# Optimization experiments

Hardware: AMD Instinct MI355X
Metric: run time of the kernel (lower is better)

The kernel has to match this reference:

```python
import jax, jax.numpy as jnp
import numpy as np

V = 25000
E = 100000
NODE_IN = 74
EDGE_IN = 12
OUT = 64
EHID = 128
NUM_STEPS = 6


def setup_inputs() -> dict:
    key = jax.random.key(0)
    ks = jax.random.split(key, 12)
    s = 0.05
    node_feats = jax.random.normal(ks[0], (V, NODE_IN), dtype=jnp.float32)
    edge_feats = jax.random.normal(ks[1], (E, EDGE_IN), dtype=jnp.float32)
    src = jax.random.randint(ks[2], (E,), 0, V)
    dst = jax.random.randint(ks[3], (E,), 0, V)
    # project_node_feats: Linear(node_in, out)
    Wp = jax.random.normal(ks[4], (NODE_IN, OUT), dtype=jnp.float32) * s
    bp = jnp.zeros((OUT,), dtype=jnp.float32)
    # edge network: Linear(edge_in, ehid) -> ReLU -> Linear(ehid, out*out)
    We1 = jax.random.normal(ks[5], (EDGE_IN, EHID), dtype=jnp.float32) * s
    be1 = jnp.zeros((EHID,), dtype=jnp.float32)
    We2 = jax.random.normal(ks[6], (EHID, OUT * OUT), dtype=jnp.float32) * s
    be2 = jnp.zeros((OUT * OUT,), dtype=jnp.float32)
    # NNConv output bias
    bias = jnp.zeros((OUT,), dtype=jnp.float32)
    return {
        "node_feats": node_feats, "edge_feats": edge_feats,
        "src": src, "dst": dst,
        "Wp": Wp, "bp": bp,
        "We1": We1, "be1": be1, "We2": We2, "be2": be2,
        "bias": bias,
    }


def reference(node_feats, edge_feats, src, dst, Wp, bp, We1, be1, We2, be2, bias):
    # project node features
    h = jax.nn.relu(node_feats @ Wp + bp)  # [V, OUT]
    # per-edge weight matrices (same every step -> hoist out of loop)
    ew = jax.nn.relu(edge_feats @ We1 + be1) @ We2 + be2  # [E, OUT*OUT]
    ew = ew.reshape(E, OUT, OUT)
    for _ in range(NUM_STEPS):
        # gather src node feats, batched matvec, scatter-sum to dst
        msg = jnp.einsum('ei,eio->eo', h[src], ew)  # [E, OUT]
        agg = jax.ops.segment_sum(msg, dst, num_segments=V)  # [V, OUT]
        h = jax.nn.relu(agg + bias)
    return h
```

## Files before the change

### kernel.cpp

```cpp
#include <hip/hip_runtime.h>
#include <hip/hip_bf16.h>

#define Vn 25000
#define En 100000
#define NODE_IN 74
#define EDGE_IN 12
#define OUTD 64
#define EHID 128
#define NUM_STEPS 6

#define EPB 64
#define HPAD 68

typedef __attribute__((ext_vector_type(8))) _Float16 half8;
typedef __attribute__((ext_vector_type(16))) float floatx16;

__global__ void proj_kernel(const float* __restrict__ node,
                            const float* __restrict__ Wp,
                            const float* __restrict__ bp,
                            float* __restrict__ h) {
  __shared__ float nf[NODE_IN];
  int v = blockIdx.x;
  int o = threadIdx.x;
  for (int i = o; i < NODE_IN; i += 64) nf[i] = node[(size_t)v * NODE_IN + i];
  __syncthreads();
  float acc = bp[o];
  for (int i = 0; i < NODE_IN; ++i) acc = fmaf(nf[i], Wp[i * OUTD + o], acc);
  h[(size_t)v * OUTD + o] = fmaxf(acc, 0.0f);
}

__global__ void edge_kernel(const float* __restrict__ ef,
                            const float* __restrict__ We1,
                            const float* __restrict__ be1,
                            _Float16* __restrict__ f) {
  __shared__ float es[EDGE_IN];
  int e = blockIdx.x;
  int k = threadIdx.x;
  if (k < EDGE_IN) es[k] = ef[(size_t)e * EDGE_IN + k];
  __syncthreads();
  float acc = be1[k];
  for (int j = 0; j < EDGE_IN; ++j) acc = fmaf(es[j], We1[j * EHID + k], acc);
  f[(size_t)e * EHID + k] = (_Float16)fmaxf(acc, 0.0f);
}

__global__ void w2r_kernel(const float* __restrict__ We2,
                           _Float16* __restrict__ w2s) {
  int g = blockIdx.x * 256 + threadIdx.x;
  int j = g & 7;
  int lane = (g >> 3) & 63;
  int s = (g >> 9) & 7;
  int c = (g >> 12) & 1;
  int i = g >> 13;
  int k = s * 16 + 8 * (lane >> 5) + j;
  int col = i * 64 + c * 32 + (lane & 31);
  w2s[g] = (_Float16)We2[(size_t)k * (OUTD * OUTD) + col];
}

__global__ __launch_bounds__(512) void msg_kernel(
    const float* __restrict__ h,
    const _Float16* __restrict__ f,
    const _Float16* __restrict__ w2s,
    const int* __restrict__ src,
    const int* __restrict__ dst,
    const float* __restrict__ be2,
    float* __restrict__ agg) {
  __shared__ _Float16 h_t[64 * HPAD];
  __shared__ float accbuf[4 * 1024];
  __shared__ int s_dst[EPB];

  const int tid = threadIdx.x;
  const int wvq = tid >> 6;
  const int eh = (wvq >> 2) & 1;
  const int ch = (wvq >> 1) & 1;
  const int kh = wvq & 1;
  const int lane = tid & 63;
  const int l31 = lane & 31;
  const int lh = lane >> 5;
  const int e0 = blockIdx.x * EPB;

  if (tid < EPB) {
    int e = e0 + tid;
    s_dst[tid] = (e < En) ? dst[e] : -1;
  }
  {
    int e = tid & 63;
    int ib = tid >> 6;
    int eg = e0 + e;
    int sv = (eg < En) ? src[eg] : 0;
    const float4* hp = reinterpret_cast<const float4*>(h + (size_t)sv * OUTD + ib * 8);
    for (int cc = 0; cc < 2; ++cc) {
      float4 val = hp[cc];
      int i4 = ib * 8 + cc * 4;
      h_t[(i4 + 0) * HPAD + e] = (_Float16)val.x;
      h_t[(i4 + 1) * HPAD + e] = (_Float16)val.y;
      h_t[(i4 + 2) * HPAD + e] = (_Float16)val.z;
      h_t[(i4 + 3) * HPAD + e] = (_Float16)val.w;
    }
  }
  __syncthreads();

  half8 afr[4];
  {
    int e = e0 + eh * 32 + l31;
    if (e >= En) e = En - 1;
    const _Float16* fr = f + (size_t)e * EHID + kh * 64 + 8 * lh;
    for (int s = 0; s < 4; ++s)
      afr[s] = *reinterpret_cast<const half8*>(fr + s * 16);
  }

  const _Float16* w2b = w2s + ch * 4096 + kh * 2048 + lane * 8;

#define LOADB(dstv, ii)                                                     \
  {                                                                         \
    const _Float16* p_ = w2b + (size_t)(ii) * 8192;                         \
    dstv[0] = *reinterpret_cast<const half8*>(p_);                          \
    dstv[1] = *reinterpret_cast<const half8*>(p_ + 512);                    \
    dstv[2] = *reinterpret_cast<const half8*>(p_ + 1024);                   \
    dstv[3] = *reinterpret_cast<const half8*>(p_ + 1536);                   \
  }

  floatx16 acc = (floatx16){0.f};

  half8 ba[4], bb[4];
  LOADB(ba, 0);
  LOADB(bb, 1);

#define BODY(iv, breg)                                                        \
  {                                                                           \
    _Float16 hh = h_t[(iv) * HPAD + eh * 32 + l31];                           \
    half8 hb = (half8){hh, hh, hh, hh, hh, hh, hh, hh};                       \
    for (int s = 0; s < 4; ++s) {                                             \
      half8 as = afr[s] * hb;                                                 \
      acc = __builtin_amdgcn_mfma_f32_32x32x16_f16(as, breg[s], acc, 0, 0, 0); \
    }                                                                         \
  }

  for (int ii = 0; ii < 32; ++ii) {
    int i0 = 2 * ii;
    BODY(i0, ba);
    {
      int inx = (i0 + 2 < 64) ? i0 + 2 : 63;
      LOADB(ba, inx);
    }
    BODY(i0 + 1, bb);
    {
      int inx = (i0 + 3 < 64) ? i0 + 3 : 63;
      LOADB(bb, inx);
    }
  }

  if (kh == 0) {
    for (int s = 0; s < 4; ++s) {
      half8 ha, b2;
      for (int j = 0; j < 8; ++j) {
        int i = s * 16 + 8 * lh + j;
        ha[j] = h_t[i * HPAD + eh * 32 + l31];
        b2[j] = (_Float16)be2[i * 64 + ch * 32 + l31];
      }
      acc = __builtin_amdgcn_mfma_f32_32x32x16_f16(ha, b2, acc, 0, 0, 0);
    }
  }

  {
    float* ab = &accbuf[(eh * 2 + ch) * 1024];
    if (kh == 1) {
      for (int reg = 0; reg < 16; ++reg) ab[reg * 64 + lane] = acc[reg];
    }
  }
  __syncthreads();
  if (kh == 0) {
    const float* ab = &accbuf[(eh * 2 + ch) * 1024];
    int col = ch * 32 + l31;
    for (int reg = 0; reg < 16; ++reg) {
      float v = acc[reg] + ab[reg * 64 + lane];
      int r = (reg & 3) + 8 * (reg >> 2) + 4 * lh;
      int d = s_dst[eh * 32 + r];
      if (d >= 0) atomicAdd(&agg[(size_t)d * OUTD + col], v);
    }
  }
}

__global__ void update_kernel(float* __restrict__ agg,
                              const float* __restrict__ bias,
                              float* __restrict__ hout,
                              float* __restrict__ dout, int last) {
  int g = blockIdx.x * 256 + threadIdx.x;
  if (g >= Vn * OUTD) return;
  float v = agg[g];
  agg[g] = 0.0f;
  float r = fmaxf(v + bias[g & 63], 0.0f);
  hout[g] = r;
  if (last) dout[g] = r;
}

extern "C" void kernel_launch(void* const* d_in, const int* in_sizes, int n_in,
                              void* d_out, int out_size, void* d_ws, size_t ws_size,
                              hipStream_t stream) {
  const float* node = (const float*)d_in[0];
  const float* edge = (const float*)d_in[1];
  const int* src = (const int*)d_in[2];
  const int* dst = (const int*)d_in[3];
  const float* Wp   = (const float*)d_in[4];
  const float* bp   = (const float*)d_in[5];
  const float* We1  = (const float*)d_in[6];
  const float* be1  = (const float*)d_in[7];
  const float* We2  = (const float*)d_in[8];
  const float* be2  = (const float*)d_in[9];
  const float* bias = (const float*)d_in[10];
  float* out = (float*)d_out;

  char* ws = (char*)d_ws;
  float* agg = (float*)(ws);
  float* h_a = (float*)(ws + 6400000);
  float* h_b = (float*)(ws + 12800000);
  _Float16* f   = (_Float16*)(ws + 19200000);
  _Float16* w2s = (_Float16*)(ws + 44800000);

  hipMemsetAsync(agg, 0, (size_t)Vn * OUTD * sizeof(float), stream);
  proj_kernel<<<Vn, 64, 0, stream>>>(node, Wp, bp, h_a);
  edge_kernel<<<En, 128, 0, stream>>>(edge, We1, be1, f);
  w2r_kernel<<<(OUTD * OUTD * EHID) / 256, 256, 0, stream>>>(We2, w2s);

  float* hin = h_a;
  float* hout = h_b;
  for (int s = 0; s < NUM_STEPS; ++s) {
    msg_kernel<<<(En + EPB - 1) / EPB, 512, 0, stream>>>(hin, f, w2s, src, dst, be2, agg);
    update_kernel<<<(Vn * OUTD + 255) / 256, 256, 0, stream>>>(
        agg, bias, hout, out, s == NUM_STEPS - 1);
    float* t = hin; hin = hout; hout = t;
  }
}
```

Baseline: 1.001 ms.

## Reuse W2 fragments across four edge tiles per wave, drop LDS K-reduction

Each block now handles 128 edges with 4 waves instead of 64 edges with 8 waves. Every wave keeps four 32-edge accumulators, so each W2 fragment it loads feeds four MFMAs instead of one, which cuts the per-block re-read of the 1MB fp16 W2 tensor. The LDS buffer that combined the two K-halves is removed, and both K-half waves now atomically add their partial sums straight to the global aggregate. That doubles the number of global atomics and raises register pressure (four accumulators plus sixteen A fragments per wave).

```diff
diff --git a/kernel.cpp b/kernel.cpp
--- a/kernel.cpp
+++ b/kernel.cpp
@@ -9,8 +9,8 @@
 #define EHID 128
 #define NUM_STEPS 6
 
-#define EPB 64
-#define HPAD 68
+#define EPB 128
+#define HPAD 132
 
 typedef __attribute__((ext_vector_type(8))) _Float16 half8;
 typedef __attribute__((ext_vector_type(16))) float floatx16;
@@ -56,7 +56,7 @@
   w2s[g] = (_Float16)We2[(size_t)k * (OUTD * OUTD) + col];
 }
 
-__global__ __launch_bounds__(512) void msg_kernel(
+__global__ __launch_bounds__(256) void msg_kernel(
     const float* __restrict__ h,
     const _Float16* __restrict__ f,
     const _Float16* __restrict__ w2s,
@@ -65,14 +65,12 @@
     const float* __restrict__ be2,
     float* __restrict__ agg) {
   __shared__ _Float16 h_t[64 * HPAD];
-  __shared__ float accbuf[4 * 1024];
   __shared__ int s_dst[EPB];
 
   const int tid = threadIdx.x;
   const int wvq = tid >> 6;
-  const int eh = (wvq >> 2) & 1;
-  const int ch = (wvq >> 1) & 1;
-  const int kh = wvq & 1;
+  const int ch = wvq & 1;
+  const int kh = wvq >> 1;
   const int lane = tid & 63;
   const int l31 = lane & 31;
   const int lh = lane >> 5;
@@ -83,14 +81,14 @@
     s_dst[tid] = (e < En) ? dst[e] : -1;
   }
   {
-    int e = tid & 63;
-    int ib = tid >> 6;
+    int e = tid & 127;
+    int ib = tid >> 7;
     int eg = e0 + e;
     int sv = (eg < En) ? src[eg] : 0;
-    const float4* hp = reinterpret_cast<const float4*>(h + (size_t)sv * OUTD + ib * 8);
-    for (int cc = 0; cc < 2; ++cc) {
+    const float4* hp = reinterpret_cast<const float4*>(h + (size_t)sv * OUTD + ib * 32);
+    for (int cc = 0; cc < 8; ++cc) {
       float4 val = hp[cc];
-      int i4 = ib * 8 + cc * 4;
+      int i4 = ib * 32 + cc * 4;
       h_t[(i4 + 0) * HPAD + e] = (_Float16)val.x;
       h_t[(i4 + 1) * HPAD + e] = (_Float16)val.y;
       h_t[(i4 + 2) * HPAD + e] = (_Float16)val.z;
@@ -99,13 +97,13 @@
   }
   __syncthreads();
 
-  half8 afr[4];
-  {
-    int e = e0 + eh * 32 + l31;
+  half8 afr[4][4];
+  for (int t = 0; t < 4; ++t) {
+    int e = e0 + t * 32 + l31;
     if (e >= En) e = En - 1;
     const _Float16* fr = f + (size_t)e * EHID + kh * 64 + 8 * lh;
     for (int s = 0; s < 4; ++s)
-      afr[s] = *reinterpret_cast<const half8*>(fr + s * 16);
+      afr[t][s] = *reinterpret_cast<const half8*>(fr + s * 16);
   }
 
   const _Float16* w2b = w2s + ch * 4096 + kh * 2048 + lane * 8;
@@ -119,20 +117,35 @@
     dstv[3] = *reinterpret_cast<const half8*>(p_ + 1536);                   \
   }
 
-  floatx16 acc = (floatx16){0.f};
+  floatx16 acc0 = (floatx16){0.f};
+  floatx16 acc1 = (floatx16){0.f};
+  floatx16 acc2 = (floatx16){0.f};
+  floatx16 acc3 = (floatx16){0.f};
 
   half8 ba[4], bb[4];
   LOADB(ba, 0);
   LOADB(bb, 1);
 
-#define BODY(iv, breg)                                                        \
-  {                                                                           \
-    _Float16 hh = h_t[(iv) * HPAD + eh * 32 + l31];                           \
-    half8 hb = (half8){hh, hh, hh, hh, hh, hh, hh, hh};                       \
-    for (int s = 0; s < 4; ++s) {                                             \
-      half8 as = afr[s] * hb;                                                 \
-      acc = __builtin_amdgcn_mfma_f32_32x32x16_f16(as, breg[s], acc, 0, 0, 0); \
-    }                                                                         \
+#define BODY(iv, breg)                                                          \
+  {                                                                             \
+    _Float16 h0 = h_t[(iv) * HPAD + 0 * 32 + l31];                              \
+    _Float16 h1 = h_t[(iv) * HPAD + 1 * 32 + l31];                              \
+    _Float16 h2 = h_t[(iv) * HPAD + 2 * 32 + l31];                              \
+    _Float16 h3 = h_t[(iv) * HPAD + 3 * 32 + l31];                              \
+    half8 hb0 = (half8){h0, h0, h0, h0, h0, h0, h0, h0};                        \
+    half8 hb1 = (half8){h1, h1, h1, h1, h1, h1, h1, h1};                        \
+    half8 hb2 = (half8){h2, h2, h2, h2, h2, h2, h2, h2};                        \
+    half8 hb3 = (half8){h3, h3, h3, h3, h3, h3, h3, h3};                        \
+    for (int s = 0; s < 4; ++s) {                                               \
+      half8 a0 = afr[0][s] * hb0;                                               \
+      half8 a1 = afr[1][s] * hb1;                                               \
+      half8 a2 = afr[2][s] * hb2;                                               \
+      half8 a3 = afr[3][s] * hb3;                                               \
+      acc0 = __builtin_amdgcn_mfma_f32_32x32x16_f16(a0, breg[s], acc0, 0, 0, 0); \
+      acc1 = __builtin_amdgcn_mfma_f32_32x32x16_f16(a1, breg[s], acc1, 0, 0, 0); \
+      acc2 = __builtin_amdgcn_mfma_f32_32x32x16_f16(a2, breg[s], acc2, 0, 0, 0); \
+      acc3 = __builtin_amdgcn_mfma_f32_32x32x16_f16(a3, breg[s], acc3, 0, 0, 0); \
+    }                                                                           \
   }
 
   for (int ii = 0; ii < 32; ++ii) {
@@ -150,32 +163,33 @@
   }
 
   if (kh == 0) {
+    half8 b2[4];
+    for (int s = 0; s < 4; ++s)
+      for (int j = 0; j < 8; ++j)
+        b2[s][j] = (_Float16)be2[(s * 16 + 8 * lh + j) * 64 + ch * 32 + l31];
     for (int s = 0; s < 4; ++s) {
-      half8 ha, b2;
+      half8 ha0, ha1, ha2, ha3;
       for (int j = 0; j < 8; ++j) {
         int i = s * 16 + 8 * lh + j;
-        ha[j] = h_t[i * HPAD + eh * 32 + l31];
-        b2[j] = (_Float16)be2[i * 64 + ch * 32 + l31];
+        ha0[j] = h_t[i * HPAD + 0 * 32 + l31];
+        ha1[j] = h_t[i * HPAD + 1 * 32 + l31];
+        ha2[j] = h_t[i * HPAD + 2 * 32 + l31];
+        ha3[j] = h_t[i * HPAD + 3 * 32 + l31];
       }
-      acc = __builtin_amdgcn_mfma_f32_32x32x16_f16(ha, b2, acc, 0, 0, 0);
-    }
-  }
-
-  {
-    float* ab = &accbuf[(eh * 2 + ch) * 1024];
-    if (kh == 1) {
-      for (int reg = 0; reg < 16; ++reg) ab[reg * 64 + lane] = acc[reg];
-    }
-  }
-  __syncthreads();
-  if (kh == 0) {
-    const float* ab = &accbuf[(eh * 2 + ch) * 1024];
-    int col = ch * 32 + l31;
+      acc0 = __builtin_amdgcn_mfma_f32_32x32x16_f16(ha0, b2[s], acc0, 0, 0, 0);
+      acc1 = __builtin_amdgcn_mfma_f32_32x32x16_f16(ha1, b2[s], acc1, 0, 0, 0);
+      acc2 = __builtin_amdgcn_mfma_f32_32x32x16_f16(ha2, b2[s], acc2, 0, 0, 0);
+      acc3 = __builtin_amdgcn_mfma_f32_32x32x16_f16(ha3, b2[s], acc3, 0, 0, 0);
+    }
+  }
+
+  int col = ch * 32 + l31;
+  floatx16 accs[4] = {acc0, acc1, acc2, acc3};
+  for (int t = 0; t < 4; ++t) {
     for (int reg = 0; reg < 16; ++reg) {
-      float v = acc[reg] + ab[reg * 64 + lane];
       int r = (reg & 3) + 8 * (reg >> 2) + 4 * lh;
-      int d = s_dst[eh * 32 + r];
-      if (d >= 0) atomicAdd(&agg[(size_t)d * OUTD + col], v);
+      int d = s_dst[t * 32 + r];
+      if (d >= 0) atomicAdd(&agg[(size_t)d * OUTD + col], accs[t][reg]);
     }
   }
 }
@@ -224,7 +238,7 @@
   float* hin = h_a;
   float* hout = h_b;
   for (int s = 0; s < NUM_STEPS; ++s) {
-    msg_kernel<<<(En + EPB - 1) / EPB, 512, 0, stream>>>(hin, f, w2s, src, dst, be2, agg);
+    msg_kernel<<<(En + EPB - 1) / EPB, 256, 0, stream>>>(hin, f, w2s, src, dst, be2, agg);
     update_kernel<<<(Vn * OUTD + 255) / 256, 256, 0, stream>>>(
         agg, bias, hout, out, s == NUM_STEPS - 1);
     float* t = hin; hin = hout; hout = t;
```

Result: faster. 934.6 us (-6.6%).
